# Optimization experiments

Hardware: AMD Instinct MI355X
Metric: run time of the kernel (lower is better)

The kernel has to match this reference:

```python
import jax, jax.numpy as jnp
import numpy as np

B, S, H = 4, 2048, 1024
NH, HD = 16, 64


def setup_inputs() -> dict:
    key = jax.random.key(0)
    ks = jax.random.split(key, 5)
    scale = 1.0 / np.sqrt(H)
    x = jax.random.normal(ks[0], (B, S, H), dtype=jnp.float32)
    w_qkv = jax.random.normal(ks[1], (H, 3 * H), dtype=jnp.float32) * scale
    b_qkv = jnp.zeros((3 * H,), dtype=jnp.float32)
    w_out = jax.random.normal(ks[2], (H, H), dtype=jnp.float32) * scale
    b_out = jnp.zeros((H,), dtype=jnp.float32)
    return {"x": x, "w_qkv": w_qkv, "b_qkv": b_qkv, "w_out": w_out, "b_out": b_out}


def reference(x, w_qkv, b_qkv, w_out, b_out):
    bsz, seq_len, hidden = x.shape
    qkv = x @ w_qkv + b_qkv  # [B,S,3H]
    q, k, v = jnp.split(qkv, 3, axis=-1)

    def heads(t):
        return t.reshape(bsz, seq_len, NH, HD).transpose(0, 2, 1, 3)  # [B,NH,S,HD]

    q, k, v = heads(q), heads(k), heads(v)
    scale = HD ** (-0.5)
    attn = jnp.einsum("bhqd,bhkd->bhqk", q, k) * scale  # [B,NH,S,S]
    causal = jnp.tril(jnp.ones((seq_len, seq_len), dtype=bool))
    attn = jnp.where(causal, attn, -jnp.inf)
    probs = jax.nn.softmax(attn, axis=-1)
    out = jnp.einsum("bhqk,bhkd->bhqd", probs, v)
    out = out.transpose(0, 2, 1, 3).reshape(bsz, seq_len, hidden)
    return out @ w_out + b_out
```

## Files before the change

### kernel.cpp

```cpp
#include <hip/hip_runtime.h>
#include <hip/hip_bf16.h>
#include <cstdint>

#define B_  4
#define S_  2048
#define H_  1024
#define NH_ 16
#define HD_ 64

using short8  = __attribute__((ext_vector_type(8))) short;
using floatx4 = __attribute__((ext_vector_type(4))) float;

__device__ __forceinline__ unsigned short f2b(float f) {
  union { float f; unsigned int u; } x; x.f = f;
  unsigned int r = x.u + 0x7fffu + ((x.u >> 16) & 1u);
  return (unsigned short)(r >> 16);
}
__device__ __forceinline__ unsigned short f2b_fast(float f) {
  union { float f; unsigned int u; } x; x.f = f;
  return (unsigned short)((x.u + 0x8000u) >> 16);
}
__device__ __forceinline__ unsigned int pack2(float a, float b) {
  return (unsigned int)f2b(a) | ((unsigned int)f2b(b) << 16);
}

__device__ __forceinline__ void async16(void* lds, const void* g) {
  __builtin_amdgcn_global_load_lds(
      (const __attribute__((address_space(1))) unsigned int*)g,
      (__attribute__((address_space(3))) unsigned int*)lds, 16, 0, 0);
}

__device__ __forceinline__ void transpose64(const float* __restrict__ in,
                                            unsigned short* __restrict__ out,
                                            int R, int C, int c0, int r0,
                                            bool qk_scale) {
  __shared__ float tile[64][65];
  int tx = threadIdx.x & 63, ty = threadIdx.x >> 6;
#pragma unroll
  for (int i = 0; i < 16; i++) {
    int row = i * 4 + ty;
    tile[row][tx] = in[(size_t)(r0 + row) * C + c0 + tx];
  }
  __syncthreads();
  int tx16 = threadIdx.x & 15, cy = threadIdx.x >> 4;
#pragma unroll
  for (int i = 0; i < 4; i++) {
    int c = i * 16 + cy;
    float s = (qk_scale && (c0 + c) < 1024) ? 0.125f : 1.0f;
    ushort4 o;
    o.x = f2b(tile[tx16 * 4 + 0][c] * s);
    o.y = f2b(tile[tx16 * 4 + 1][c] * s);
    o.z = f2b(tile[tx16 * 4 + 2][c] * s);
    o.w = f2b(tile[tx16 * 4 + 3][c] * s);
    *(ushort4*)&out[(size_t)(c0 + c) * R + r0 + tx16 * 4] = o;
  }
}

__global__ void k_prep(const float* __restrict__ x, const float* __restrict__ w_qkv,
                       const float* __restrict__ w_out,
                       unsigned short* __restrict__ xb, unsigned short* __restrict__ wqkvT,
                       unsigned short* __restrict__ woutT) {
  int bx = blockIdx.x, tid = threadIdx.x;
  if (bx < 2048) {
    size_t base = ((size_t)bx * 256 + tid) * 4;
    const size_t stride = (size_t)2048 * 256 * 4;
#pragma unroll
    for (int i = 0; i < 4; i++) {
      size_t idx = base + (size_t)i * stride;
      float4 v = *(const float4*)(x + idx);
      ushort4 o;
      o.x = f2b(v.x); o.y = f2b(v.y); o.z = f2b(v.z); o.w = f2b(v.w);
      *(ushort4*)(xb + idx) = o;
    }
  } else if (bx < 2048 + 768) {
    int t = bx - 2048;
    transpose64(w_qkv, wqkvT, H_, 3 * H_, (t % 48) * 64, (t / 48) * 64, true);
  } else {
    int t = bx - 2048 - 768;
    transpose64(w_out, woutT, H_, H_, (t & 15) * 64, (t >> 4) * 64, false);
  }
}

template <bool OUT_BF16>
__global__ __launch_bounds__(256, 2) void k_gemm_bt64(
    const unsigned short* __restrict__ A,
    const unsigned short* __restrict__ BT,
    const float* __restrict__ bias,
    void* __restrict__ Cout,
    unsigned short* __restrict__ vt,
    int M, int N, int K) {
  __shared__ __align__(16) unsigned short As[2][128 * 64];
  __shared__ __align__(16) unsigned short Bs[2][128 * 64];
  const int tid  = threadIdx.x;
  const int lane = tid & 63, wave = tid >> 6;
  const int quad = lane >> 4, l16 = lane & 15;
  const int wm = wave >> 1, wn = wave & 1;
  const int m0 = blockIdx.y * 128, n0 = blockIdx.x * 128;

  floatx4 acc[4][4];
#pragma unroll
  for (int mt = 0; mt < 4; mt++)
#pragma unroll
    for (int nt = 0; nt < 4; nt++)
      acc[mt][nt] = (floatx4){0.f, 0.f, 0.f, 0.f};

  auto stage = [&](int k0, int bufi) {
#pragma unroll
    for (int j = 0; j < 4; j++) {
      int c = j * 256 + tid;
      int row = c >> 3, c8 = (c & 7) ^ (row & 7);
      async16(&As[bufi][c * 8], &A[(size_t)(m0 + row) * K + k0 + c8 * 8]);
    }
#pragma unroll
    for (int j = 0; j < 4; j++) {
      int c = j * 256 + tid;
      int row = c >> 3, c8 = (c & 7) ^ (row & 7);
      async16(&Bs[bufi][c * 8], &BT[(size_t)(n0 + row) * K + k0 + c8 * 8]);
    }
  };

  stage(0, 0);
  int it = 0;
  for (int k0 = 0; k0 < K; k0 += 64, it++) {
    const int cur = it & 1;
    __syncthreads();
    if (k0 + 64 < K) stage(k0 + 64, cur ^ 1);
    short8 af[4][2], bq[4][2];
#pragma unroll
    for (int t = 0; t < 4; t++) {
      int ra = wm * 64 + t * 16 + l16;
      int rb = wn * 64 + t * 16 + l16;
#pragma unroll
      for (int ks = 0; ks < 2; ks++) {
        af[t][ks] = *(const short8*)&As[cur][(ra * 8 + ((ks * 4 + quad) ^ (ra & 7))) * 8];
        bq[t][ks] = *(const short8*)&Bs[cur][(rb * 8 + ((ks * 4 + quad) ^ (rb & 7))) * 8];
      }
    }
#pragma unroll
    for (int ks = 0; ks < 2; ks++)
#pragma unroll
      for (int mt = 0; mt < 4; mt++)
#pragma unroll
        for (int nt = 0; nt < 4; nt++)
          acc[mt][nt] = __builtin_amdgcn_mfma_f32_16x16x32_bf16(af[mt][ks], bq[nt][ks], acc[mt][nt], 0, 0, 0);
  }

  if (OUT_BF16 && n0 >= 2048) {
#pragma unroll
    for (int mt = 0; mt < 4; mt++) {
      int row0 = m0 + wm * 64 + mt * 16 + quad * 4;
      int b = row0 >> 11, s = row0 & 2047;
#pragma unroll
      for (int nt = 0; nt < 4; nt++) {
        int col = n0 + wn * 64 + nt * 16 + l16;
        float bv = bias[col];
        uint2 u;
        u.x = pack2(acc[mt][nt][0] + bv, acc[mt][nt][1] + bv);
        u.y = pack2(acc[mt][nt][2] + bv, acc[mt][nt][3] + bv);
        *(uint2*)&vt[(size_t)(b * 1024 + (col - 2048)) * S_ + s] = u;
      }
    }
  } else {
#pragma unroll
    for (int mt = 0; mt < 4; mt++) {
      int row = m0 + wm * 64 + mt * 16 + quad * 4;
#pragma unroll
      for (int nt = 0; nt < 4; nt++) {
        int col = n0 + wn * 64 + nt * 16 + l16;
        float bv = bias[col];
        if (OUT_BF16 && col < 1024) bv *= 0.125f;
#pragma unroll
        for (int r = 0; r < 4; r++) {
          float v = acc[mt][nt][r] + bv;
          if (OUT_BF16) ((unsigned short*)Cout)[(size_t)(row + r) * N + col] = f2b(v);
          else          ((float*)Cout)[(size_t)(row + r) * N + col] = v;
        }
      }
    }
  }
}

__global__ __launch_bounds__(256, 3) void k_attn(
    const unsigned short* __restrict__ qkv,
    const unsigned short* __restrict__ vt,
    unsigned short* __restrict__ outb) {
  __shared__ __align__(16) unsigned short Ks [2][64 * 64];
  __shared__ __align__(16) unsigned short VTs[2][64 * 64];
  __shared__ __align__(16) unsigned short Ps[4][16 * 64];

  const int tid  = threadIdx.x;
  const int lane = tid & 63, w = tid >> 6;
  const int quad = lane >> 4, l16 = lane & 15;
  const int qt = (S_ / 128 - 1) - (blockIdx.x >> 6);
  const int bh = blockIdx.x & 63;
  const int b = bh >> 4, h = bh & 15;
  const int qwv = qt * 128 + w * 32;
  const int wv2 = w & 1;

  short8 qf[2][2];
  for (int g = 0; g < 2; g++)
    for (int kh = 0; kh < 2; kh++)
      qf[g][kh] = *(const short8*)&qkv[(size_t)(b * S_ + qwv + g * 16 + l16) * (3 * H_)
                                       + h * HD_ + kh * 32 + quad * 8];

  floatx4 oacc[2][4];
  float lsum[2] = {0.f, 0.f};
  for (int g = 0; g < 2; g++)
    for (int ct = 0; ct < 4; ct++) oacc[g][ct] = (floatx4){0.f, 0.f, 0.f, 0.f};

  auto stage = [&](int kt, int bufi) {
    if (w < 2) {
      for (int j = 0; j < 4; j++) {
        int c = wv2 * 256 + j * 64 + lane;
        int row = c >> 3, c8 = (c & 7) ^ (row & 7);
        async16(&Ks[bufi][c * 8],
                &qkv[(size_t)(b * S_ + kt * 64 + row) * (3 * H_) + H_ + h * HD_ + c8 * 8]);
      }
    } else {
      for (int j = 0; j < 4; j++) {
        int c = wv2 * 256 + j * 64 + lane;
        int row = c >> 3, c8 = (c & 7) ^ (row & 7);
        async16(&VTs[bufi][c * 8],
                &vt[(size_t)(bh * HD_ + row) * S_ + kt * 64 + c8 * 8]);
      }
    }
  };

  unsigned short* Pw = &Ps[w][0];

  const int ktmax = 2 * qt + 1;
  stage(0, 0);
  for (int kt = 0; kt <= ktmax; kt++) {
    const int cur = kt & 1;
    __syncthreads();
    if (kt < ktmax) stage(kt + 1, cur ^ 1);

    if (kt * 64 <= qwv + 31) {
      const bool need_mask = (kt * 64 + 63 > qwv);

      short8 vf[4][2];
      for (int ct = 0; ct < 4; ct++)
        for (int kh = 0; kh < 2; kh++) {
          int vrow = ct * 16 + l16;
          vf[ct][kh] = *(const short8*)&VTs[cur][(vrow * 8 + ((kh * 4 + quad) ^ (vrow & 7))) * 8];
        }

      uint2 pk[2][4];
      for (int ct = 0; ct < 4; ct++) {
        int krow = ct * 16 + l16;
        short8 kf0 = *(const short8*)&Ks[cur][(krow * 8 + ((0 + quad) ^ (krow & 7))) * 8];
        short8 kf1 = *(const short8*)&Ks[cur][(krow * 8 + ((4 + quad) ^ (krow & 7))) * 8];
        for (int g = 0; g < 2; g++) {
          floatx4 z = (floatx4){0.f, 0.f, 0.f, 0.f};
          z = __builtin_amdgcn_mfma_f32_16x16x32_bf16(kf0, qf[g][0], z, 0, 0, 0);
          z = __builtin_amdgcn_mfma_f32_16x16x32_bf16(kf1, qf[g][1], z, 0, 0, 0);
          float p[4];
          if (need_mask) {
            int kvb = kt * 64 + ct * 16 + quad * 4;
            int q = qwv + g * 16 + l16;
            for (int r = 0; r < 4; r++)
              p[r] = (kvb + r <= q) ? __expf(z[r]) : 0.f;
          } else {
            for (int r = 0; r < 4; r++) p[r] = __expf(z[r]);
          }
          lsum[g] += (p[0] + p[1]) + (p[2] + p[3]);
          pk[g][ct].x = (unsigned int)f2b_fast(p[0]) | ((unsigned int)f2b_fast(p[1]) << 16);
          pk[g][ct].y = (unsigned int)f2b_fast(p[2]) | ((unsigned int)f2b_fast(p[3]) << 16);
        }
      }

      for (int g = 0; g < 2; g++) {
        for (int ct = 0; ct < 4; ct++) {
          int slot = (ct * 2 + (quad >> 1)) ^ (l16 & 7);
          *(uint2*)&Pw[l16 * 64 + slot * 8 + (quad & 1) * 4] = pk[g][ct];
        }
        for (int kh = 0; kh < 2; kh++) {
          short8 pf = *(const short8*)&Pw[l16 * 64 + ((kh * 4 + quad) ^ (l16 & 7)) * 8];
          for (int ct = 0; ct < 4; ct++)
            oacc[g][ct] = __builtin_amdgcn_mfma_f32_16x16x32_bf16(vf[ct][kh], pf, oacc[g][ct], 0, 0, 0);
        }
      }
    }
  }

  for (int g = 0; g < 2; g++) {
    lsum[g] += __shfl_xor(lsum[g], 16);
    lsum[g] += __shfl_xor(lsum[g], 32);
  }

  for (int g = 0; g < 2; g++) {
    float inv = 1.0f / lsum[g];
    int q = qwv + g * 16 + l16;
    for (int ct = 0; ct < 4; ct++) {
      uint2 u;
      u.x = pack2(oacc[g][ct][0] * inv, oacc[g][ct][1] * inv);
      u.y = pack2(oacc[g][ct][2] * inv, oacc[g][ct][3] * inv);
      *(uint2*)&outb[(size_t)(b * S_ + q) * H_ + h * HD_ + ct * 16 + quad * 4] = u;
    }
  }
}

extern "C" void kernel_launch(void* const* d_in, const int* in_sizes, int n_in,
                              void* d_out, int out_size, void* d_ws, size_t ws_size,
                              hipStream_t stream) {
  const float* x     = (const float*)d_in[0];
  const float* w_qkv = (const float*)d_in[1];
  const float* b_qkv = (const float*)d_in[2];
  const float* w_out = (const float*)d_in[3];
  const float* b_out = (const float*)d_in[4];

  char* ws = (char*)d_ws;
  size_t off = 0;
  auto alloc = [&](size_t bytes) -> void* {
    void* p = ws + off;
    off = (off + bytes + 255) & ~(size_t)255;
    return p;
  };
  unsigned short* xb    = (unsigned short*)alloc((size_t)B_ * S_ * H_ * 2);
  unsigned short* wqkvT = (unsigned short*)alloc((size_t)3 * H_ * H_ * 2);
  unsigned short* woutT = (unsigned short*)alloc((size_t)H_ * H_ * 2);
  unsigned short* qkv   = (unsigned short*)alloc((size_t)B_ * S_ * 3 * H_ * 2);
  unsigned short* ao    = (unsigned short*)alloc((size_t)B_ * S_ * H_ * 2);
  unsigned short* vtb   = (unsigned short*)alloc((size_t)B_ * NH_ * HD_ * S_ * 2);

  k_prep<<<2048 + 768 + 256, 256, 0, stream>>>(x, w_qkv, w_out, xb, wqkvT, woutT);

  k_gemm_bt64<true ><<<dim3(3 * H_ / 128, B_ * S_ / 128), 256, 0, stream>>>(
      xb, wqkvT, b_qkv, qkv, vtb, B_ * S_, 3 * H_, H_);

  k_attn<<<(S_ / 128) * 64, 256, 0, stream>>>(qkv, vtb, ao);

  k_gemm_bt64<false><<<dim3(H_ / 128, B_ * S_ / 128), 256, 0, stream>>>(
      ao, woutT, b_out, (float*)d_out, nullptr, B_ * S_, H_, H_);
}
```

Before: 241.0 us.

## Use triple-buffered K=32 GEMM for the QKV projection

Adds a new GEMM kernel for the QKV projection. It uses 32-wide K tiles with a three-stage async LDS pipeline in place of 64-wide double buffering, and a launch bound that targets 3 blocks per CU. Staging work is split so waves 0-1 load A and waves 2-3 load B. The aim is better latency hiding and occupancy, at the cost of twice as many barriers per K step. The output GEMM still uses the old kernel.

```diff
diff --git a/kernel.cpp b/kernel.cpp
--- a/kernel.cpp
+++ b/kernel.cpp
@@ -78,6 +78,110 @@
   } else {
     int t = bx - 2048 - 768;
     transpose64(w_out, woutT, H_, H_, (t & 15) * 64, (t >> 4) * 64, false);
+  }
+}
+
+template <bool OUT_BF16>
+__global__ __launch_bounds__(256, 3) void k_gemm_bt32p(
+    const unsigned short* __restrict__ A,
+    const unsigned short* __restrict__ BT,
+    const float* __restrict__ bias,
+    void* __restrict__ Cout,
+    unsigned short* __restrict__ vt,
+    int M, int N, int K) {
+  __shared__ __align__(16) unsigned short As[3][128 * 32];
+  __shared__ __align__(16) unsigned short Bs[3][128 * 32];
+  const int tid  = threadIdx.x;
+  const int lane = tid & 63, wave = tid >> 6;
+  const int quad = lane >> 4, l16 = lane & 15;
+  const int wm = wave >> 1, wn = wave & 1;
+  const int m0 = blockIdx.y * 128, n0 = blockIdx.x * 128;
+  const int wv2 = wave & 1;
+
+  const unsigned short* srcbase = (wave < 2) ? A : BT;
+  const int base0 = (wave < 2) ? m0 : n0;
+
+  floatx4 acc[4][4];
+#pragma unroll
+  for (int mt = 0; mt < 4; mt++)
+#pragma unroll
+    for (int nt = 0; nt < 4; nt++)
+      acc[mt][nt] = (floatx4){0.f, 0.f, 0.f, 0.f};
+
+  auto stage = [&](int k0, int bufi) {
+    unsigned short* dst = (wave < 2) ? &As[bufi][0] : &Bs[bufi][0];
+#pragma unroll
+    for (int j = 0; j < 4; j++) {
+      int c = wv2 * 256 + j * 64 + lane;
+      int row = c >> 2, slot = c & 3;
+      int c8 = slot ^ ((row >> 1) & 3);
+      async16(&dst[c * 8], &srcbase[(size_t)(base0 + row) * K + k0 + c8 * 8]);
+    }
+  };
+
+  const int NT = K >> 5;
+  stage(0, 0);
+  stage(32, 1);
+  asm volatile("s_waitcnt vmcnt(4)" ::: "memory");
+  __builtin_amdgcn_s_barrier();
+  __builtin_amdgcn_sched_barrier(0);
+
+  for (int t = 0; t < NT; t++) {
+    const int cur = t % 3;
+    if (t + 2 < NT) stage((t + 2) * 32, (t + 2) % 3);
+    short8 af[4], bq[4];
+#pragma unroll
+    for (int tt = 0; tt < 4; tt++) {
+      int ra = wm * 64 + tt * 16 + l16;
+      int rb = wn * 64 + tt * 16 + l16;
+      af[tt] = *(const short8*)&As[cur][(ra * 4 + (quad ^ ((ra >> 1) & 3))) * 8];
+      bq[tt] = *(const short8*)&Bs[cur][(rb * 4 + (quad ^ ((rb >> 1) & 3))) * 8];
+    }
+#pragma unroll
+    for (int mt = 0; mt < 4; mt++)
+#pragma unroll
+      for (int nt = 0; nt < 4; nt++)
+        acc[mt][nt] = __builtin_amdgcn_mfma_f32_16x16x32_bf16(af[mt], bq[nt], acc[mt][nt], 0, 0, 0);
+    if (t + 1 < NT) {
+      if (t + 2 < NT) asm volatile("s_waitcnt vmcnt(4)" ::: "memory");
+      else            asm volatile("s_waitcnt vmcnt(0)" ::: "memory");
+      __builtin_amdgcn_s_barrier();
+      __builtin_amdgcn_sched_barrier(0);
+    }
+  }
+
+  if (OUT_BF16 && n0 >= 2048) {
+#pragma unroll
+    for (int mt = 0; mt < 4; mt++) {
+      int row0 = m0 + wm * 64 + mt * 16 + quad * 4;
+      int b = row0 >> 11, s = row0 & 2047;
+#pragma unroll
+      for (int nt = 0; nt < 4; nt++) {
+        int col = n0 + wn * 64 + nt * 16 + l16;
+        float bv = bias[col];
+        uint2 u;
+        u.x = pack2(acc[mt][nt][0] + bv, acc[mt][nt][1] + bv);
+        u.y = pack2(acc[mt][nt][2] + bv, acc[mt][nt][3] + bv);
+        *(uint2*)&vt[(size_t)(b * 1024 + (col - 2048)) * S_ + s] = u;
+      }
+    }
+  } else {
+#pragma unroll
+    for (int mt = 0; mt < 4; mt++) {
+      int row = m0 + wm * 64 + mt * 16 + quad * 4;
+#pragma unroll
+      for (int nt = 0; nt < 4; nt++) {
+        int col = n0 + wn * 64 + nt * 16 + l16;
+        float bv = bias[col];
+        if (OUT_BF16 && col < 1024) bv *= 0.125f;
+#pragma unroll
+        for (int r = 0; r < 4; r++) {
+          float v = acc[mt][nt][r] + bv;
+          if (OUT_BF16) ((unsigned short*)Cout)[(size_t)(row + r) * N + col] = f2b(v);
+          else          ((float*)Cout)[(size_t)(row + r) * N + col] = v;
+        }
+      }
+    }
   }
 }
 
@@ -325,7 +429,7 @@
 
   k_prep<<<2048 + 768 + 256, 256, 0, stream>>>(x, w_qkv, w_out, xb, wqkvT, woutT);
 
-  k_gemm_bt64<true ><<<dim3(3 * H_ / 128, B_ * S_ / 128), 256, 0, stream>>>(
+  k_gemm_bt32p<true ><<<dim3(3 * H_ / 128, B_ * S_ / 128), 256, 0, stream>>>(
       xb, wqkvT, b_qkv, qkv, vtb, B_ * S_, 3 * H_, H_);
 
   k_attn<<<(S_ / 128) * 64, 256, 0, stream>>>(qkv, vtb, ao);
```

New measurement: 259.1 us. 7.5% more time.
